# Kernel tuning notes

Measured on AMD Instinct MI355X. Metric: run time of the kernel, lower is better.

Reference implementation:

```python
import jax, jax.numpy as jnp
from jax import lax
import numpy as np

KK = 9          # 3x3 kernel points
BN_EPS = 1e-5


def setup_inputs() -> dict:
    key = jax.random.key(0)
    ks = jax.random.split(key, 8)
    B, C, O, H, W = 4, 256, 256, 64, 64
    x = jax.random.normal(ks[0], (B, C, H, W), jnp.float32)
    # offset/mask conv: 27 = 2*9 offsets + 9 mask logits; small init so offsets are O(1) px
    w_off = jax.random.normal(ks[1], (3 * KK, C, 3, 3), jnp.float32) * 0.01
    b_off = jnp.zeros((3 * KK,), jnp.float32)
    # main deformable conv weight [O, C, 3, 3]
    w = jax.random.normal(ks[2], (O, C, 3, 3), jnp.float32) * (1.0 / np.sqrt(C * KK))
    b = jax.random.normal(ks[3], (O,), jnp.float32) * 0.01
    # BatchNorm (eval mode) params
    gamma = jax.random.uniform(ks[4], (O,), jnp.float32, 0.5, 1.5)
    beta = jax.random.normal(ks[5], (O,), jnp.float32) * 0.1
    running_mean = jax.random.normal(ks[6], (O,), jnp.float32) * 0.1
    running_var = jax.random.uniform(ks[7], (O,), jnp.float32, 0.5, 1.5)
    return dict(x=x, w_off=w_off, b_off=b_off, w=w, b=b, gamma=gamma,
                beta=beta, running_mean=running_mean, running_var=running_var)


def _bilinear_sample(x, py, px):
    """x: [B,C,H,W]; py/px: [B,KK,H,W] float sample coords -> [B,C,KK,H,W]."""
    B, C, H, W = x.shape
    xflat = x.reshape(B, C, H * W)
    y0 = jnp.floor(py)
    x0 = jnp.floor(px)
    ly = py - y0      # frac weights
    lx = px - x0
    y0i = y0.astype(jnp.int32)
    x0i = x0.astype(jnp.int32)

    def corner(yi, xi, wgt):
        valid = (yi >= 0) & (yi < H) & (xi >= 0) & (xi < W)  # zero padding outside
        idx = jnp.clip(yi, 0, H - 1) * W + jnp.clip(xi, 0, W - 1)
        v = jnp.take_along_axis(xflat, idx.reshape(B, 1, -1), axis=2)  # [B,C,KK*H*W]
        return v * (wgt * valid).reshape(B, 1, -1)

    out = (corner(y0i,     x0i,     (1 - ly) * (1 - lx))
           + corner(y0i,     x0i + 1, (1 - ly) * lx)
           + corner(y0i + 1, x0i,     ly * (1 - lx))
           + corner(y0i + 1, x0i + 1, ly * lx))
    return out.reshape(B, C, KK, H, W)


def _deform_conv_bn_relu(x, w_off, b_off, w, b, gamma, beta, running_mean, running_var):
    B, C, H, W = x.shape
    O = w.shape[0]
    # offset/mask branch: plain 3x3 conv, stride 1, pad 1
    om = lax.conv_general_dilated(x, w_off, (1, 1), [(1, 1), (1, 1)])
    om = om + b_off[None, :, None, None]              # [B, 27, H, W]
    off_y = om[:, :KK]                                # DCNv2: o1 -> y offsets
    off_x = om[:, KK:2 * KK]                          # o2 -> x offsets
    mask = jax.nn.sigmoid(om[:, 2 * KK:])             # [B, 9, H, W]

    # base sampling grid for each of the 9 kernel taps (stride 1, pad 1)
    k = jnp.arange(KK)
    ki = (k // 3)[None, :, None, None].astype(jnp.float32)
    kj = (k % 3)[None, :, None, None].astype(jnp.float32)
    hh = jnp.arange(H, dtype=jnp.float32)[None, None, :, None]
    ww = jnp.arange(W, dtype=jnp.float32)[None, None, None, :]
    py = hh - 1.0 + ki + off_y                        # [B,9,H,W]
    px = ww - 1.0 + kj + off_x

    sampled = _bilinear_sample(x, py, px)             # [B,C,9,H,W]
    sampled = sampled * mask[:, None]                 # modulated (DCNv2)

    out = jnp.einsum('bckhw,ock->bohw', sampled, w.reshape(O, C, KK))
    out = out + b[None, :, None, None]

    # BatchNorm (eval / running stats) + ReLU
    inv = gamma / jnp.sqrt(running_var + BN_EPS)
    out = out * inv[None, :, None, None] + (beta - running_mean * inv)[None, :, None, None]
    return jax.nn.relu(out)


def reference(x, w_off, b_off, w, b, gamma, beta, running_mean, running_var):
    return _deform_conv_bn_relu(x, w_off, b_off, w, b, gamma, beta,
                                running_mean, running_var)
```

## Files before the change

kernel.cpp:

```cpp
#include <hip/hip_runtime.h>

#define HH 64
#define WWD 64
#define CIN 256
#define OUTC 256
#define BB 4
#define KK 9
#define NSO2 18
#define QOFF 4
#define NITH 20
#define WROWS 8
#define WPIX 512

typedef __attribute__((ext_vector_type(8))) short short8;
typedef __attribute__((ext_vector_type(4))) short short4v;
typedef __attribute__((ext_vector_type(4))) unsigned short ushort4v;
typedef __attribute__((ext_vector_type(4))) float float4v;

__device__ __forceinline__ short f2bf(float f) {
    unsigned u = __builtin_bit_cast(unsigned, f);
    u += 0x7fffu + ((u >> 16) & 1u);
    return (short)(u >> 16);
}
__device__ __forceinline__ float bf2f(short s) {
    unsigned u = ((unsigned)(unsigned short)s) << 16;
    return __builtin_bit_cast(float, u);
}
__device__ __forceinline__ unsigned cvtpk(float a, float b) {
    unsigned r;
    asm("v_cvt_pk_bf16_f32 %0, %1, %2" : "=v"(r) : "v"(a), "v"(b));
    return r;
}
__device__ __forceinline__ short8 pack8(const float* a) {
    union { short8 s; unsigned u[4]; } r;
    r.u[0] = cvtpk(a[0], a[1]); r.u[1] = cvtpk(a[2], a[3]);
    r.u[2] = cvtpk(a[4], a[5]); r.u[3] = cvtpk(a[6], a[7]);
    return r.s;
}
__device__ __forceinline__ int div9(int s) { return (s * 57) >> 9; }

__global__ __launch_bounds__(256) void k_packs(const float* __restrict__ w,
                                               const float* __restrict__ w_off,
                                               short* __restrict__ wt2,
                                               short* __restrict__ wo2) {
    const int bid = blockIdx.x;
    if (bid < 2304) {
        int gid = bid * 256 + threadIdx.x;
        int kk = gid & 31;
        int o  = (gid >> 5) & 255;
        int s  = gid >> 13;
        int chunk = div9(s), tap = s - 9 * chunk;
        int c = (chunk << 5) + kk;
        wt2[gid] = f2bf(w[(o * CIN + c) * 9 + tap]);
    } else {
        int gid = (bid - 2304) * 256 + threadIdx.x;
        int kk = gid & 31;
        int m  = (gid >> 5) & 31;
        int s  = gid >> 10;
        int chunk = div9(s), tap = s - 9 * chunk;
        int c = (chunk << 5) + kk;
        wo2[gid] = (m < 27) ? f2bf(w_off[(m * CIN + c) * 9 + tap]) : (short)0;
    }
}

__global__ __launch_bounds__(256) void k_off_mfma(const float* __restrict__ x,
                                                  const short* __restrict__ wo2,
                                                  float* __restrict__ om_part) {
    const int wgid = blockIdx.x;
    const int swz  = ((wgid & 7) << 7) + (wgid >> 3);
    const int q = swz & 3;
    const int h = (swz >> 2) & 63;
    const int b = swz >> 8;
    const int tid = threadIdx.x;
    const int lane = tid & 63;
    const int wid  = tid >> 6;

    __shared__ short S[2][4][64][8];

    const int px_t = tid & 63;
    const int g    = tid >> 6;
    const float* xb = x + ((size_t)b << 20);

    float gv[8];
    auto ISSUE = [&](int s2) {
        const int chunk = div9(s2), tap = s2 - 9 * chunk;
        const int gy = h + tap / 3 - 1;
        const int gx = px_t + tap % 3 - 1;
        const bool ok = ((unsigned)gy < 64u) && ((unsigned)gx < 64u);
        const float* xc = xb + (((chunk << 5) + (g << 3)) << 12) + (gy << 6) + gx;
#pragma unroll
        for (int j = 0; j < 8; ++j)
            gv[j] = ok ? xc[(size_t)j << 12] : 0.f;
    };
    auto CONSUME = [&](int buf) {
        short8 p = pack8(gv);
        *(short8*)(&S[buf][g][px_t][0]) = p;
    };

    const int arow = lane & 15;
    const int akk  = (lane >> 4) << 3;
    const int bpx  = lane & 15;
    const int bg   = lane >> 4;

    float4v acc0 = {0.f, 0.f, 0.f, 0.f};
    float4v acc1 = {0.f, 0.f, 0.f, 0.f};

    const int s0 = q * NSO2;
    ISSUE(s0); CONSUME(0); ISSUE(s0 + 1);
    const short* abase = wo2 + (size_t)s0 * 1024 + arow * 32 + akk;
    short8 aC0 = *(const short8*)(abase);
    short8 aC1 = *(const short8*)(abase + 512);
    __syncthreads();

#pragma unroll 1
    for (int ls = 0; ls < NSO2; ++ls) {
        const int lsn = (ls + 1 < NSO2) ? ls + 1 : ls;
        const short* an = wo2 + (size_t)(s0 + lsn) * 1024 + arow * 32 + akk;
        short8 aN0 = *(const short8*)(an);
        short8 aN1 = *(const short8*)(an + 512);

        short8 bf = *(const short8*)(&S[ls & 1][bg][(wid << 4) + bpx][0]);
        acc0 = __builtin_amdgcn_mfma_f32_16x16x32_bf16(aC0, bf, acc0, 0, 0, 0);
        acc1 = __builtin_amdgcn_mfma_f32_16x16x32_bf16(aC1, bf, acc1, 0, 0, 0);

        if (ls < NSO2 - 1) {
            CONSUME((ls + 1) & 1);
            if (ls + 2 < NSO2) ISSUE(s0 + ls + 2);
        }
        aC0 = aN0; aC1 = aN1;
        __syncthreads();
    }

    const int pxo = (wid << 4) + bpx;
    float* ob = om_part + (((size_t)(q * BB + b) * 27) << 12) + (h << 6) + pxo;
#pragma unroll
    for (int r = 0; r < 4; ++r) {
        const int m0 = ((lane >> 4) << 2) + r;
        ob[(size_t)m0 << 12] = acc0[r];
        const int m1 = 16 + m0;
        if (m1 < 27) ob[(size_t)m1 << 12] = acc1[r];
    }
}

__global__ __launch_bounds__(512) void k_main(
    const float* __restrict__ x, const float* __restrict__ om_part,
    const float* __restrict__ b_off, const short* __restrict__ wt2,
    float* __restrict__ outr, float* __restrict__ part1) {

    const int wgid = blockIdx.x;
    const int swz  = ((wgid & 7) << 6) + (wgid >> 3);
    const int q = swz & 1;
    const int h = (swz >> 1) & 63;
    const int b = swz >> 7;
    const int tid  = threadIdx.x;
    const int lane = tid & 63;
    const int wid  = tid >> 6;

    __shared__ ushort4v sidx2[576];
    __shared__ ushort4v sw4[576];
    __shared__ short    S[2][2][4][64][8];
    __shared__ short    xw[WPIX * 32];

    for (int j = tid; j < 576; j += 512) {
        const int k  = j >> 6;
        const int px = j & 63;
        const int sp = (h << 6) + px;
        float oy = b_off[k], ox = b_off[k + KK], mz = b_off[k + 2 * KK];
#pragma unroll
        for (int qq = 0; qq < QOFF; ++qq) {
            const float* bp = om_part + (size_t)((qq * BB + b) * 27) * 4096 + sp;
            oy += bp[k * 4096];
            ox += bp[(k + KK) * 4096];
            mz += bp[(k + 2 * KK) * 4096];
        }
        const float mask = 1.f / (1.f + expf(-mz));
        const float py  = (float)h  - 1.f + (float)(k / 3) + oy;
        const float pxc = (float)px - 1.f + (float)(k % 3) + ox;
        const float y0f = floorf(py), x0f = floorf(pxc);
        const float ly = py - y0f, lx = pxc - x0f;
        const int y0 = (int)y0f, x0 = (int)x0f;

        float w00, w01, w10, w11;
        {
            bool v = (y0 >= 0) && (y0 < HH) && (x0 >= 0) && (x0 < WWD);
            w00 = v ? (1.f - ly) * (1.f - lx) * mask : 0.f;
        }
        {
            bool v = (y0 >= 0) && (y0 < HH) && (x0 + 1 < WWD) && (x0 + 1 >= 0);
            w01 = v ? (1.f - ly) * lx * mask : 0.f;
        }
        {
            bool v = (y0 + 1 >= 0) && (y0 + 1 < HH) && (x0 >= 0) && (x0 < WWD);
            w10 = v ? ly * (1.f - lx) * mask : 0.f;
        }
        {
            bool v = (y0 + 1 >= 0) && (y0 + 1 < HH) && (x0 + 1 >= 0) && (x0 + 1 < WWD);
            w11 = v ? ly * lx * mask : 0.f;
        }
        const int cy0 = min(max(y0, 0), 63),     cy1 = min(max(y0 + 1, 0), 63);
        const int cx0 = min(max(x0, 0), 63),     cx1 = min(max(x0 + 1, 0), 63);
        const int li0 = cy0 - (h - 3),           li1 = cy1 - (h - 3);
        ushort4v pv;
        if ((unsigned)li0 < (unsigned)WROWS && (unsigned)li1 < (unsigned)WROWS) {
            const int p00 = (li0 << 6) + cx0, p01 = (li0 << 6) + cx1;
            const int p10 = (li1 << 6) + cx0, p11 = (li1 << 6) + cx1;
            pv.x = (unsigned short)((p00 << 6) | ((p00 + (p00 >> 2)) & 3));
            pv.y = (unsigned short)((p01 << 6) | ((p01 + (p01 >> 2)) & 3));
            pv.z = (unsigned short)((p10 << 6) | ((p10 + (p10 >> 2)) & 3));
            pv.w = (unsigned short)((p11 << 6) | ((p11 + (p11 >> 2)) & 3));
        } else {
            pv.x = 0xFFFFu;
            pv.y = (unsigned short)(y0 + 32);
            pv.z = (unsigned short)(x0 + 32);
            pv.w = 0;
        }
        ushort4v wv;
        wv.x = (unsigned short)f2bf(w00);
        wv.y = (unsigned short)f2bf(w01);
        wv.z = (unsigned short)f2bf(w10);
        wv.w = (unsigned short)f2bf(w11);
        sidx2[j] = pv;
        sw4[j]   = wv;
    }

    const float* xb = x + ((size_t)b << 20);

    auto STAGE = [&](int chunk) {
#pragma unroll
        for (int r4 = 0; r4 < 4; ++r4) {
            const int t   = r4 * 512 + tid;
            const int g   = t >> 9;
            const int pix = t & 511;
            const int wr  = pix >> 6, col = pix & 63;
            const int gro = (min(max(h - 3 + wr, 0), 63) << 6) + col;
            const float* xc = xb + ((size_t)((chunk << 5) + (g << 3)) << 12) + gro;
            float a[8];
#pragma unroll
            for (int j = 0; j < 8; ++j) a[j] = xc[(size_t)j << 12];
            short8 p = pack8(a);
            const int pos = (g + pix + (pix >> 2)) & 3;
            *(short8*)&xw[pix * 32 + pos * 8] = p;
        }
    };

    auto SAMPLE = [&](int c2, int sub2, int ntaps2, int buf2) {
        const int tp = tid >> 8;
        if (tp < ntaps2) {
            const int slot = tid & 255;
            const int g  = slot >> 6;
            const int px = slot & 63;
            const int tap = sub2 * 2 + tp;
            const int j = (tap << 6) + px;
            const ushort4v sv = sidx2[j];
            const ushort4v wv = sw4[j];
            const float w00 = bf2f((short)wv.x), w01 = bf2f((short)wv.y);
            const float w10 = bf2f((short)wv.z), w11 = bf2f((short)wv.w);
            float a[8];
            if (sv.x != 0xFFFFu) {
                const int o0 = ((sv.x & 0xFFC0u) >> 1) + (((sv.x + g) & 3u) << 3);
                const int o1 = ((sv.y & 0xFFC0u) >> 1) + (((sv.y + g) & 3u) << 3);
                const int o2 = ((sv.z & 0xFFC0u) >> 1) + (((sv.z + g) & 3u) << 3);
                const int o3 = ((sv.w & 0xFFC0u) >> 1) + (((sv.w + g) & 3u) << 3);
                const short8 c00 = *(const short8*)&xw[o0];
                const short8 c01 = *(const short8*)&xw[o1];
                const short8 c10 = *(const short8*)&xw[o2];
                const short8 c11 = *(const short8*)&xw[o3];
#pragma unroll
                for (int j2 = 0; j2 < 8; ++j2)
                    a[j2] = w00 * bf2f(c00[j2]) + w01 * bf2f(c01[j2])
                          + w10 * bf2f(c10[j2]) + w11 * bf2f(c11[j2]);
            } else {
                const int y0 = (int)sv.y - 32, x0 = (int)sv.z - 32;
                const int cy0 = min(max(y0, 0), 63), cy1 = min(max(y0 + 1, 0), 63);
                const int cx0 = min(max(x0, 0), 63), cx1 = min(max(x0 + 1, 0), 63);
                const int i00 = (cy0 << 6) + cx0, i01 = (cy0 << 6) + cx1;
                const int i10 = (cy1 << 6) + cx0, i11 = (cy1 << 6) + cx1;
                const float* xc = xb + ((size_t)((c2 << 5) + (g << 3)) << 12);
#pragma unroll
                for (int j2 = 0; j2 < 8; ++j2) {
                    a[j2] = w00 * xc[i00] + w01 * xc[i01]
                          + w10 * xc[i10] + w11 * xc[i11];
                    xc += 4096;
                }
            }
            short8 rr = pack8(a);
            *(short8*)&S[buf2][tp][g][px][0] = rr;
        }
    };

    const short* wbase = wt2 + ((wid * 32 + (lane & 15)) << 5) + ((lane >> 4) << 3);
    const int bpx = lane & 15;
    const int bg  = lane >> 4;

    float4v acc[2][4];
#pragma unroll
    for (int mt = 0; mt < 2; ++mt)
#pragma unroll
        for (int nt = 0; nt < 4; ++nt) acc[mt][nt] = (float4v){0.f, 0.f, 0.f, 0.f};

    const int c0 = q * 4;
    const int sA0 = c0 * 9;

    __syncthreads();
    STAGE(c0);
    __syncthreads();
    SAMPLE(c0, 0, 2, 0);
    short8 aC00 = *(const short8*)(wbase + (size_t)sA0 * 8192);
    short8 aC01 = *(const short8*)(wbase + (size_t)sA0 * 8192 + 512);
    short8 aC10 = *(const short8*)(wbase + (size_t)(sA0 + 1) * 8192);
    short8 aC11 = *(const short8*)(wbase + (size_t)(sA0 + 1) * 8192 + 512);
    __syncthreads();

    int c = c0, sub = 0;
#pragma unroll 1
    for (int it = 0; it < NITH; ++it) {
        const int ntaps = (sub < 4) ? 2 : 1;
        int subn = sub + 1, cn = c;
        if (subn == 5) { subn = 0; cn = c + 1; }
        const int ntapsN = (subn < 4) ? 2 : 1;
        const int sN = cn * 9 + subn * 2;

        short8 aN00 = aC00, aN01 = aC01, aN10 = aC10, aN11 = aC11;
        if (it + 1 < NITH) {
            aN00 = *(const short8*)(wbase + (size_t)sN * 8192);
            aN01 = *(const short8*)(wbase + (size_t)sN * 8192 + 512);
            if (ntapsN == 2) {
                aN10 = *(const short8*)(wbase + (size_t)(sN + 1) * 8192);
                aN11 = *(const short8*)(wbase + (size_t)(sN + 1) * 8192 + 512);
            }
        }

        const int buf = it & 1;
        __builtin_amdgcn_s_setprio(1);
        {
            const short* Sb = &S[buf][0][bg][bpx][0];
            short8 b0 = *(const short8*)(Sb);
            short8 b1 = *(const short8*)(Sb + 128);
            short8 b2 = *(const short8*)(Sb + 256);
            short8 b3 = *(const short8*)(Sb + 384);
            acc[0][0] = __builtin_amdgcn_mfma_f32_16x16x32_bf16(aC00, b0, acc[0][0], 0, 0, 0);
            acc[0][1] = __builtin_amdgcn_mfma_f32_16x16x32_bf16(aC00, b1, acc[0][1], 0, 0, 0);
            acc[0][2] = __builtin_amdgcn_mfma_f32_16x16x32_bf16(aC00, b2, acc[0][2], 0, 0, 0);
            acc[0][3] = __builtin_amdgcn_mfma_f32_16x16x32_bf16(aC00, b3, acc[0][3], 0, 0, 0);
            acc[1][0] = __builtin_amdgcn_mfma_f32_16x16x32_bf16(aC01, b0, acc[1][0], 0, 0, 0);
            acc[1][1] = __builtin_amdgcn_mfma_f32_16x16x32_bf16(aC01, b1, acc[1][1], 0, 0, 0);
            acc[1][2] = __builtin_amdgcn_mfma_f32_16x16x32_bf16(aC01, b2, acc[1][2], 0, 0, 0);
            acc[1][3] = __builtin_amdgcn_mfma_f32_16x16x32_bf16(aC01, b3, acc[1][3], 0, 0, 0);
        }
        if (ntaps == 2) {
            const short* Sb = &S[buf][1][bg][bpx][0];
            short8 b0 = *(const short8*)(Sb);
            short8 b1 = *(const short8*)(Sb + 128);
            short8 b2 = *(const short8*)(Sb + 256);
            short8 b3 = *(const short8*)(Sb + 384);
            acc[0][0] = __builtin_amdgcn_mfma_f32_16x16x32_bf16(aC10, b0, acc[0][0], 0, 0, 0);
            acc[0][1] = __builtin_amdgcn_mfma_f32_16x16x32_bf16(aC10, b1, acc[0][1], 0, 0, 0);
            acc[0][2] = __builtin_amdgcn_mfma_f32_16x16x32_bf16(aC10, b2, acc[0][2], 0, 0, 0);
            acc[0][3] = __builtin_amdgcn_mfma_f32_16x16x32_bf16(aC10, b3, acc[0][3], 0, 0, 0);
            acc[1][0] = __builtin_amdgcn_mfma_f32_16x16x32_bf16(aC11, b0, acc[1][0], 0, 0, 0);
            acc[1][1] = __builtin_amdgcn_mfma_f32_16x16x32_bf16(aC11, b1, acc[1][1], 0, 0, 0);
            acc[1][2] = __builtin_amdgcn_mfma_f32_16x16x32_bf16(aC11, b2, acc[1][2], 0, 0, 0);
            acc[1][3] = __builtin_amdgcn_mfma_f32_16x16x32_bf16(aC11, b3, acc[1][3], 0, 0, 0);
        }
        __builtin_amdgcn_s_setprio(0);

        if (it + 1 < NITH) {
            if (sub == 4) {
                STAGE(cn);
                __syncthreads();
            }
            SAMPLE(cn, subn, ntapsN, (it + 1) & 1);
        }
        aC00 = aN00; aC01 = aN01; aC10 = aN10; aC11 = aN11;
        __syncthreads();
        c = cn; sub = subn;
    }

    const int r4 = lane >> 4;
    float* ob = (q == 0 ? outr : part1) + (((size_t)b * 256) << 12) + (h << 6);
#pragma unroll
    for (int mt = 0; mt < 2; ++mt)
#pragma unroll
        for (int nt = 0; nt < 4; ++nt) {
            const int px = nt * 16 + bpx;
#pragma unroll
            for (int r = 0; r < 4; ++r) {
                const int o = wid * 32 + mt * 16 + r4 * 4 + r;
                ob[((size_t)o << 12) + px] = acc[mt][nt][r];
            }
        }
}

__global__ __launch_bounds__(256) void k_bn(const float* __restrict__ part1,
                                            const float* __restrict__ bias,
                                            const float* __restrict__ gamma,
                                            const float* __restrict__ beta,
                                            const float* __restrict__ rmean,
                                            const float* __restrict__ rvar,
                                            float* __restrict__ out) {
    const int NTOT4 = BB * OUTC * 4096 / 4;
    int i = blockIdx.x * 256 + threadIdx.x;
    const int stride = gridDim.x * 256;
#pragma unroll 1
    for (; i < NTOT4; i += stride) {
        const int e0 = i << 2;
        const int o  = (e0 >> 12) & 255;
        const float inv = gamma[o] * rsqrtf(rvar[o] + 1e-5f);
        const float sh  = beta[o] - rmean[o] * inv + bias[o] * inv;
        float4 a = ((const float4*)out)[i];
        float4 p = ((const float4*)part1)[i];
        float4 v;
        v.x = fmaxf((a.x + p.x) * inv + sh, 0.f);
        v.y = fmaxf((a.y + p.y) * inv + sh, 0.f);
        v.z = fmaxf((a.z + p.z) * inv + sh, 0.f);
        v.w = fmaxf((a.w + p.w) * inv + sh, 0.f);
        ((float4*)out)[i] = v;
    }
}

extern "C" void kernel_launch(void* const* d_in, const int* in_sizes, int n_in,
                              void* d_out, int out_size, void* d_ws, size_t ws_size,
                              hipStream_t stream) {
    const float* x     = (const float*)d_in[0];
    const float* w_off = (const float*)d_in[1];
    const float* b_off = (const float*)d_in[2];
    const float* w     = (const float*)d_in[3];
    const float* bias  = (const float*)d_in[4];
    const float* gamma = (const float*)d_in[5];
    const float* beta  = (const float*)d_in[6];
    const float* rmean = (const float*)d_in[7];
    const float* rvar  = (const float*)d_in[8];
    float* out = (float*)d_out;

    float* om_part = (float*)d_ws;
    short* wt2     = (short*)(om_part + QOFF * BB * 27 * 4096);
    short* wo2     = wt2 + 72 * 256 * 32;
    float* part1   = (float*)(wo2 + 72 * 32 * 32);

    k_packs<<<2592, 256, 0, stream>>>(w, w_off, wt2, wo2);
    k_off_mfma<<<1024, 256, 0, stream>>>(x, wo2, om_part);
    k_main<<<512, 512, 0, stream>>>(x, om_part, b_off, wt2, out, part1);
    k_bn<<<2048, 256, 0, stream>>>(part1, bias, gamma, beta, rmean, rvar, out);
}
```

Baseline: 71.81 us.

## Process three taps per iteration and drop weight-fragment prefetch

Changes the main loop from five sub-steps per chunk (2,2,2,2,1 taps) to three sub-steps of three taps each, cutting the iteration count and the number of barriers per chunk. Sampling now does 768 tasks per step over 512 threads, so half the threads do two tasks, which is uneven. The register-level prefetch of the next iteration's weight fragments is removed and the weights are loaded at the start of each iteration. This may expose global-load latency but frees registers, and the S buffer grows to hold three taps.

After: 71.18 us. Within noise of the previous version (-0.9%).

```diff
diff --git a/kernel.cpp b/kernel.cpp
--- a/kernel.cpp
+++ b/kernel.cpp
@@ -8,7 +8,7 @@
 #define KK 9
 #define NSO2 18
 #define QOFF 4
-#define NITH 20
+#define NIT3 12
 #define WROWS 8
 #define WPIX 512
 
@@ -158,7 +158,7 @@
 
     __shared__ ushort4v sidx2[576];
     __shared__ ushort4v sw4[576];
-    __shared__ short    S[2][2][4][64][8];
+    __shared__ short    S[2][3][4][64][8];
     __shared__ short    xw[WPIX * 32];
 
     for (int j = tid; j < 576; j += 512) {
@@ -243,49 +243,51 @@
         }
     };
 
-    auto SAMPLE = [&](int c2, int sub2, int ntaps2, int buf2) {
-        const int tp = tid >> 8;
-        if (tp < ntaps2) {
-            const int slot = tid & 255;
-            const int g  = slot >> 6;
-            const int px = slot & 63;
-            const int tap = sub2 * 2 + tp;
-            const int j = (tap << 6) + px;
-            const ushort4v sv = sidx2[j];
-            const ushort4v wv = sw4[j];
-            const float w00 = bf2f((short)wv.x), w01 = bf2f((short)wv.y);
-            const float w10 = bf2f((short)wv.z), w11 = bf2f((short)wv.w);
-            float a[8];
-            if (sv.x != 0xFFFFu) {
-                const int o0 = ((sv.x & 0xFFC0u) >> 1) + (((sv.x + g) & 3u) << 3);
-                const int o1 = ((sv.y & 0xFFC0u) >> 1) + (((sv.y + g) & 3u) << 3);
-                const int o2 = ((sv.z & 0xFFC0u) >> 1) + (((sv.z + g) & 3u) << 3);
-                const int o3 = ((sv.w & 0xFFC0u) >> 1) + (((sv.w + g) & 3u) << 3);
-                const short8 c00 = *(const short8*)&xw[o0];
-                const short8 c01 = *(const short8*)&xw[o1];
-                const short8 c10 = *(const short8*)&xw[o2];
-                const short8 c11 = *(const short8*)&xw[o3];
-#pragma unroll
-                for (int j2 = 0; j2 < 8; ++j2)
-                    a[j2] = w00 * bf2f(c00[j2]) + w01 * bf2f(c01[j2])
-                          + w10 * bf2f(c10[j2]) + w11 * bf2f(c11[j2]);
-            } else {
-                const int y0 = (int)sv.y - 32, x0 = (int)sv.z - 32;
-                const int cy0 = min(max(y0, 0), 63), cy1 = min(max(y0 + 1, 0), 63);
-                const int cx0 = min(max(x0, 0), 63), cx1 = min(max(x0 + 1, 0), 63);
-                const int i00 = (cy0 << 6) + cx0, i01 = (cy0 << 6) + cx1;
-                const int i10 = (cy1 << 6) + cx0, i11 = (cy1 << 6) + cx1;
-                const float* xc = xb + ((size_t)((c2 << 5) + (g << 3)) << 12);
-#pragma unroll
-                for (int j2 = 0; j2 < 8; ++j2) {
-                    a[j2] = w00 * xc[i00] + w01 * xc[i01]
-                          + w10 * xc[i10] + w11 * xc[i11];
-                    xc += 4096;
-                }
+    auto TASK = [&](int c2, int sub2, int t, int buf2) {
+        const int tp   = t >> 8;
+        const int slot = t & 255;
+        const int g  = slot >> 6;
+        const int px = slot & 63;
+        const int tap = sub2 * 3 + tp;
+        const int j = (tap << 6) + px;
+        const ushort4v sv = sidx2[j];
+        const ushort4v wv = sw4[j];
+        const float w00 = bf2f((short)wv.x), w01 = bf2f((short)wv.y);
+        const float w10 = bf2f((short)wv.z), w11 = bf2f((short)wv.w);
+        float a[8];
+        if (sv.x != 0xFFFFu) {
+            const int o0 = ((sv.x & 0xFFC0u) >> 1) + (((sv.x + g) & 3u) << 3);
+            const int o1 = ((sv.y & 0xFFC0u) >> 1) + (((sv.y + g) & 3u) << 3);
+            const int o2 = ((sv.z & 0xFFC0u) >> 1) + (((sv.z + g) & 3u) << 3);
+            const int o3 = ((sv.w & 0xFFC0u) >> 1) + (((sv.w + g) & 3u) << 3);
+            const short8 c00 = *(const short8*)&xw[o0];
+            const short8 c01 = *(const short8*)&xw[o1];
+            const short8 c10 = *(const short8*)&xw[o2];
+            const short8 c11 = *(const short8*)&xw[o3];
+#pragma unroll
+            for (int j2 = 0; j2 < 8; ++j2)
+                a[j2] = w00 * bf2f(c00[j2]) + w01 * bf2f(c01[j2])
+                      + w10 * bf2f(c10[j2]) + w11 * bf2f(c11[j2]);
+        } else {
+            const int y0 = (int)sv.y - 32, x0 = (int)sv.z - 32;
+            const int cy0 = min(max(y0, 0), 63), cy1 = min(max(y0 + 1, 0), 63);
+            const int cx0 = min(max(x0, 0), 63), cx1 = min(max(x0 + 1, 0), 63);
+            const int i00 = (cy0 << 6) + cx0, i01 = (cy0 << 6) + cx1;
+            const int i10 = (cy1 << 6) + cx0, i11 = (cy1 << 6) + cx1;
+            const float* xc = xb + ((size_t)((c2 << 5) + (g << 3)) << 12);
+#pragma unroll
+            for (int j2 = 0; j2 < 8; ++j2) {
+                a[j2] = w00 * xc[i00] + w01 * xc[i01]
+                      + w10 * xc[i10] + w11 * xc[i11];
+                xc += 4096;
             }
-            short8 rr = pack8(a);
-            *(short8*)&S[buf2][tp][g][px][0] = rr;
-        }
+        }
+        short8 rr = pack8(a);
+        *(short8*)&S[buf2][tp][g][px][0] = rr;
+    };
+    auto SAMPLE3 = [&](int c2, int sub2, int buf2) {
+        TASK(c2, sub2, tid, buf2);
+        if (tid < 256) TASK(c2, sub2, 512 + tid, buf2);
     };
 
     const short* wbase = wt2 + ((wid * 32 + (lane & 15)) << 5) + ((lane >> 4) << 3);
@@ -299,36 +301,23 @@
         for (int nt = 0; nt < 4; ++nt) acc[mt][nt] = (float4v){0.f, 0.f, 0.f, 0.f};
 
     const int c0 = q * 4;
-    const int sA0 = c0 * 9;
 
     __syncthreads();
     STAGE(c0);
     __syncthreads();
-    SAMPLE(c0, 0, 2, 0);
-    short8 aC00 = *(const short8*)(wbase + (size_t)sA0 * 8192);
-    short8 aC01 = *(const short8*)(wbase + (size_t)sA0 * 8192 + 512);
-    short8 aC10 = *(const short8*)(wbase + (size_t)(sA0 + 1) * 8192);
-    short8 aC11 = *(const short8*)(wbase + (size_t)(sA0 + 1) * 8192 + 512);
+    SAMPLE3(c0, 0, 0);
     __syncthreads();
 
     int c = c0, sub = 0;
 #pragma unroll 1
-    for (int it = 0; it < NITH; ++it) {
-        const int ntaps = (sub < 4) ? 2 : 1;
-        int subn = sub + 1, cn = c;
-        if (subn == 5) { subn = 0; cn = c + 1; }
-        const int ntapsN = (subn < 4) ? 2 : 1;
-        const int sN = cn * 9 + subn * 2;
-
-        short8 aN00 = aC00, aN01 = aC01, aN10 = aC10, aN11 = aC11;
-        if (it + 1 < NITH) {
-            aN00 = *(const short8*)(wbase + (size_t)sN * 8192);
-            aN01 = *(const short8*)(wbase + (size_t)sN * 8192 + 512);
-            if (ntapsN == 2) {
-                aN10 = *(const short8*)(wbase + (size_t)(sN + 1) * 8192);
-                aN11 = *(const short8*)(wbase + (size_t)(sN + 1) * 8192 + 512);
-            }
-        }
+    for (int it = 0; it < NIT3; ++it) {
+        const int sbase = c * 9 + sub * 3;
+        const short8 a00 = *(const short8*)(wbase + (size_t)sbase * 8192);
+        const short8 a01 = *(const short8*)(wbase + (size_t)sbase * 8192 + 512);
+        const short8 a10 = *(const short8*)(wbase + (size_t)(sbase + 1) * 8192);
+        const short8 a11 = *(const short8*)(wbase + (size_t)(sbase + 1) * 8192 + 512);
+        const short8 a20 = *(const short8*)(wbase + (size_t)(sbase + 2) * 8192);
+        const short8 a21 = *(const short8*)(wbase + (size_t)(sbase + 2) * 8192 + 512);
 
         const int buf = it & 1;
         __builtin_amdgcn_s_setprio(1);
@@ -338,42 +327,58 @@
             short8 b1 = *(const short8*)(Sb + 128);
             short8 b2 = *(const short8*)(Sb + 256);
             short8 b3 = *(const short8*)(Sb + 384);
-            acc[0][0] = __builtin_amdgcn_mfma_f32_16x16x32_bf16(aC00, b0, acc[0][0], 0, 0, 0);
-            acc[0][1] = __builtin_amdgcn_mfma_f32_16x16x32_bf16(aC00, b1, acc[0][1], 0, 0, 0);
-            acc[0][2] = __builtin_amdgcn_mfma_f32_16x16x32_bf16(aC00, b2, acc[0][2], 0, 0, 0);
-            acc[0][3] = __builtin_amdgcn_mfma_f32_16x16x32_bf16(aC00, b3, acc[0][3], 0, 0, 0);
-            acc[1][0] = __builtin_amdgcn_mfma_f32_16x16x32_bf16(aC01, b0, acc[1][0], 0, 0, 0);
-            acc[1][1] = __builtin_amdgcn_mfma_f32_16x16x32_bf16(aC01, b1, acc[1][1], 0, 0, 0);
-            acc[1][2] = __builtin_amdgcn_mfma_f32_16x16x32_bf16(aC01, b2, acc[1][2], 0, 0, 0);
-            acc[1][3] = __builtin_amdgcn_mfma_f32_16x16x32_bf16(aC01, b3, acc[1][3], 0, 0, 0);
-        }
-        if (ntaps == 2) {
+            acc[0][0] = __builtin_amdgcn_mfma_f32_16x16x32_bf16(a00, b0, acc[0][0], 0, 0, 0);
+            acc[0][1] = __builtin_amdgcn_mfma_f32_16x16x32_bf16(a00, b1, acc[0][1], 0, 0, 0);
+            acc[0][2] = __builtin_amdgcn_mfma_f32_16x16x32_bf16(a00, b2, acc[0][2], 0, 0, 0);
+            acc[0][3] = __builtin_amdgcn_mfma_f32_16x16x32_bf16(a00, b3, acc[0][3], 0, 0, 0);
+            acc[1][0] = __builtin_amdgcn_mfma_f32_16x16x32_bf16(a01, b0, acc[1][0], 0, 0, 0);
+            acc[1][1] = __builtin_amdgcn_mfma_f32_16x16x32_bf16(a01, b1, acc[1][1], 0, 0, 0);
+            acc[1][2] = __builtin_amdgcn_mfma_f32_16x16x32_bf16(a01, b2, acc[1][2], 0, 0, 0);
+            acc[1][3] = __builtin_amdgcn_mfma_f32_16x16x32_bf16(a01, b3, acc[1][3], 0, 0, 0);
+        }
+        {
             const short* Sb = &S[buf][1][bg][bpx][0];
             short8 b0 = *(const short8*)(Sb);
             short8 b1 = *(const short8*)(Sb + 128);
             short8 b2 = *(const short8*)(Sb + 256);
             short8 b3 = *(const short8*)(Sb + 384);
-            acc[0][0] = __builtin_amdgcn_mfma_f32_16x16x32_bf16(aC10, b0, acc[0][0], 0, 0, 0);
-            acc[0][1] = __builtin_amdgcn_mfma_f32_16x16x32_bf16(aC10, b1, acc[0][1], 0, 0, 0);
-            acc[0][2] = __builtin_amdgcn_mfma_f32_16x16x32_bf16(aC10, b2, acc[0][2], 0, 0, 0);
-            acc[0][3] = __builtin_amdgcn_mfma_f32_16x16x32_bf16(aC10, b3, acc[0][3], 0, 0, 0);
-            acc[1][0] = __builtin_amdgcn_mfma_f32_16x16x32_bf16(aC11, b0, acc[1][0], 0, 0, 0);
-            acc[1][1] = __builtin_amdgcn_mfma_f32_16x16x32_bf16(aC11, b1, acc[1][1], 0, 0, 0);
-            acc[1][2] = __builtin_amdgcn_mfma_f32_16x16x32_bf16(aC11, b2, acc[1][2], 0, 0, 0);
-            acc[1][3] = __builtin_amdgcn_mfma_f32_16x16x32_bf16(aC11, b3, acc[1][3], 0, 0, 0);
+            acc[0][0] = __builtin_amdgcn_mfma_f32_16x16x32_bf16(a10, b0, acc[0][0], 0, 0, 0);
+            acc[0][1] = __builtin_amdgcn_mfma_f32_16x16x32_bf16(a10, b1, acc[0][1], 0, 0, 0);
+            acc[0][2] = __builtin_amdgcn_mfma_f32_16x16x32_bf16(a10, b2, acc[0][2], 0, 0, 0);
+            acc[0][3] = __builtin_amdgcn_mfma_f32_16x16x32_bf16(a10, b3, acc[0][3], 0, 0, 0);
+            acc[1][0] = __builtin_amdgcn_mfma_f32_16x16x32_bf16(a11, b0, acc[1][0], 0, 0, 0);
+            acc[1][1] = __builtin_amdgcn_mfma_f32_16x16x32_bf16(a11, b1, acc[1][1], 0, 0, 0);
+            acc[1][2] = __builtin_amdgcn_mfma_f32_16x16x32_bf16(a11, b2, acc[1][2], 0, 0, 0);
+            acc[1][3] = __builtin_amdgcn_mfma_f32_16x16x32_bf16(a11, b3, acc[1][3], 0, 0, 0);
+        }
+        {
+            const short* Sb = &S[buf][2][bg][bpx][0];
+            short8 b0 = *(const short8*)(Sb);
+            short8 b1 = *(const short8*)(Sb + 128);
+            short8 b2 = *(const short8*)(Sb + 256);
+            short8 b3 = *(const short8*)(Sb + 384);
+            acc[0][0] = __builtin_amdgcn_mfma_f32_16x16x32_bf16(a20, b0, acc[0][0], 0, 0, 0);
+            acc[0][1] = __builtin_amdgcn_mfma_f32_16x16x32_bf16(a20, b1, acc[0][1], 0, 0, 0);
+            acc[0][2] = __builtin_amdgcn_mfma_f32_16x16x32_bf16(a20, b2, acc[0][2], 0, 0, 0);
+            acc[0][3] = __builtin_amdgcn_mfma_f32_16x16x32_bf16(a20, b3, acc[0][3], 0, 0, 0);
+            acc[1][0] = __builtin_amdgcn_mfma_f32_16x16x32_bf16(a21, b0, acc[1][0], 0, 0, 0);
+            acc[1][1] = __builtin_amdgcn_mfma_f32_16x16x32_bf16(a21, b1, acc[1][1], 0, 0, 0);
+            acc[1][2] = __builtin_amdgcn_mfma_f32_16x16x32_bf16(a21, b2, acc[1][2], 0, 0, 0);
+            acc[1][3] = __builtin_amdgcn_mfma_f32_16x16x32_bf16(a21, b3, acc[1][3], 0, 0, 0);
         }
         __builtin_amdgcn_s_setprio(0);
 
-        if (it + 1 < NITH) {
-            if (sub == 4) {
+        if (it + 1 < NIT3) {
+            int subn = sub + 1, cn = c;
+            if (subn == 3) { subn = 0; cn = c + 1; }
+            if (subn == 0) {
                 STAGE(cn);
                 __syncthreads();
             }
-            SAMPLE(cn, subn, ntapsN, (it + 1) & 1);
-        }
-        aC00 = aN00; aC01 = aN01; aC10 = aN10; aC11 = aN11;
+            SAMPLE3(cn, subn, (it + 1) & 1);
+            c = cn; sub = subn;
+        }
         __syncthreads();
-        c = cn; sub = subn;
     }
 
     const int r4 = lane >> 4;
```
